# Kernel optimization log

Measured on AMD Instinct MI355X. Metric: run time of the kernel, lower is better.

Reference implementation:

```python
import jax, jax.numpy as jnp
import numpy as np


def _mlp(h, W_in, b_in, W_hid, b_hid, W_out, b_out):
    # 392 -> 1000 -> (1000)x4 -> 392, ReLU between linear layers (NICE shift net)
    h = jax.nn.relu(h @ W_in + b_in)
    for i in range(W_hid.shape[0]):  # fixed small layer count, not a data dim
        h = jax.nn.relu(h @ W_hid[i] + b_hid[i])
    return h @ W_out + b_out


def setup_inputs() -> dict:
    key = jax.random.key(0)
    ks = jax.random.split(key, 4)
    B, D, MID = 4096, 784, 1000
    half = D // 2
    return {
        "x": jax.random.normal(ks[0], (B, D), jnp.float32),
        "log_det_J": jnp.zeros((1,), jnp.float32),
        "W_in": jax.random.normal(ks[1], (half, MID), jnp.float32) * 0.05,
        "b_in": jnp.zeros((MID,), jnp.float32),
        "W_hid": jax.random.normal(ks[2], (4, MID, MID), jnp.float32) * 0.03,
        "b_hid": jnp.zeros((4, MID), jnp.float32),
        "W_out": jax.random.normal(ks[3], (MID, half), jnp.float32) * 0.03,
        "b_out": jnp.zeros((half,), jnp.float32),
    }


def reference(x, log_det_J, W_in, b_in, W_hid, b_hid, W_out, b_out):
    # mask_config = 0: first = even columns, second = odd columns
    first = x[:, 0::2]   # (B, D/2)
    second = x[:, 1::2]  # (B, D/2)
    shift = _mlp(first, W_in, b_in, W_hid, b_hid, W_out, b_out)
    y_second = second + shift  # coupling_law (reverse=False)
    # interleave: y[:, 0::2] = first, y[:, 1::2] = y_second, in one strided write
    y = jnp.stack([first, y_second], axis=2).reshape(x.shape)
    return (y, log_det_J)
```

## Files before the change

kernel.cpp:

```cpp
#include <hip/hip_runtime.h>

typedef __bf16 bf16;
typedef __bf16 bf16x8 __attribute__((ext_vector_type(8)));
typedef float f32x4 __attribute__((ext_vector_type(4)));

#define M_TOT 4096
#define D_IN  784
#define HALF  392
#define MID   1000
#define K0PAD 448
#define NPAD  1024

__device__ __forceinline__ void g2l16(const bf16* g, bf16* l) {
  __builtin_amdgcn_global_load_lds(
      (__attribute__((address_space(1))) void*)(g),
      (__attribute__((address_space(3))) void*)(l),
      16, 0, 0);
}

__device__ __forceinline__ void wtrans_tile(const float* __restrict__ W, bf16* __restrict__ WT,
                                            int K, int N, int Kpad, int tn, int tk,
                                            float (*tb)[33], int tid) {
  int n0 = tn * 32, k0 = tk * 32;
  int tx = tid & 31, ty = tid >> 5;
#pragma unroll
  for (int r = 0; r < 4; ++r) {
    int k = k0 + ty + 8 * r, n = n0 + tx;
    tb[ty + 8 * r][tx] = (k < K && n < N) ? W[(size_t)k * N + n] : 0.f;
  }
  __syncthreads();
#pragma unroll
  for (int r = 0; r < 4; ++r) {
    int n = n0 + ty + 8 * r, k = k0 + tx;
    WT[(size_t)n * Kpad + k] = (bf16)tb[tx][ty + 8 * r];
  }
}

__global__ void prep_k(const float* __restrict__ x, const float* __restrict__ ldj,
                       const float* __restrict__ W_in,
                       bf16* __restrict__ A0, bf16* __restrict__ WT0,
                       float* __restrict__ y) {
  __shared__ float tb[32][33];
  const int b = blockIdx.x, tid = threadIdx.x;
  if (b < 896) {
    int g = b * 256 + tid;
    int m = g / 56;
    int kq = g - m * 56, k0 = kq * 8;
    bf16x8 v;
    if (k0 < HALF) {
      const float4* xr = (const float4*)(x + (size_t)m * D_IN + 2 * k0);
      float4 a0 = xr[0], a1 = xr[1], a2 = xr[2], a3 = xr[3];
      v[0] = (bf16)a0.x; v[1] = (bf16)a0.z;
      v[2] = (bf16)a1.x; v[3] = (bf16)a1.z;
      v[4] = (bf16)a2.x; v[5] = (bf16)a2.z;
      v[6] = (bf16)a3.x; v[7] = (bf16)a3.z;
    } else {
#pragma unroll
      for (int j = 0; j < 8; ++j) v[j] = (bf16)0.f;
    }
    *(bf16x8*)(A0 + (size_t)m * K0PAD + k0) = v;
    if (b == 0 && tid == 0) y[(size_t)M_TOT * D_IN] = ldj[0];
    return;
  }
  int u = b - 896;
  wtrans_tile(W_in, WT0, HALF, MID, K0PAD, u & 31, u >> 5, tb, tid);
}

template <int BM, int BN, int EPI, int K>
__global__ __launch_bounds__(256, 2)
void gemm_k(const bf16* __restrict__ A, const bf16* __restrict__ BT,
            const float* __restrict__ bias, int bias_n,
            bf16* __restrict__ C,
            const float* __restrict__ x, float* __restrict__ y, int nb,
            const float* __restrict__ Wx, bf16* __restrict__ WTx,
            int wK, int wN, int wKpad, int wTN) {
  constexpr int BK = 64;
  constexpr int MT = BM / 32, NT = BN / 32;
  constexpr int KT = K / BK;
  constexpr int NBM = M_TOT / BM;
  constexpr int AI = (BM / 4) / 8;
  constexpr int BI = (BN / 4) / 8;
  constexpr int LPS = AI + BI;
  static_assert(K % BK == 0 && KT >= 2, "K/BK");
  alignas(16) __shared__ bf16 ldsA[2][BM * BK];
  alignas(16) __shared__ bf16 ldsB[2][BN * BK];
  const int tid = threadIdx.x;
  const int id = blockIdx.x;

  if (id >= nb) {
    int u = id - nb;
    wtrans_tile(Wx, WTx, wK, wN, wKpad, u % wTN, u / wTN, (float(*)[33])&ldsA[0][0], tid);
    return;
  }

  const int wave = tid >> 6, lane = tid & 63;
  const int bm = id % NBM, bn = id / NBM;

  const int srow = lane >> 3;
  const int scol = lane & 7;
  const bf16* gAb = A + ((size_t)bm * BM + wave * (BM / 4)) * K;
  const bf16* gBb = BT + ((size_t)bn * BN + wave * (BN / 4)) * K;
  const int lAo = wave * (BM / 4) * BK;
  const int lBo = wave * (BN / 4) * BK;

  const int mlane = lane & 15, quad = lane >> 4;
  const int wm = (wave & 1) * (BM / 2), wn = (wave >> 1) * (BN / 2);
  const int axor = mlane & 7;

  auto stage = [&](int kt, int pb) {
    const int koff = kt * BK;
#pragma unroll
    for (int i = 0; i < AI; ++i) {
      int r = i * 8 + srow;
      g2l16(gAb + (size_t)r * K + koff + (scol ^ (r & 7)) * 8,
            &ldsA[pb][lAo + i * 8 * BK]);
    }
#pragma unroll
    for (int i = 0; i < BI; ++i) {
      int r = i * 8 + srow;
      g2l16(gBb + (size_t)r * K + koff + (scol ^ (r & 7)) * 8,
            &ldsB[pb][lBo + i * 8 * BK]);
    }
  };

  f32x4 acc[MT][NT] = {};

  stage(0, 0);
  stage(1, 1);

  for (int kt = 0; kt < KT; ++kt) {
    const int pb = kt & 1;
    if (kt + 1 < KT)
      asm volatile("s_waitcnt vmcnt(%0)" ::"n"(LPS) : "memory");
    else
      asm volatile("s_waitcnt vmcnt(0)" ::: "memory");
    __builtin_amdgcn_s_barrier();
    __builtin_amdgcn_sched_barrier(0);

    const bf16* raB = &ldsA[pb][(wm + mlane) * BK];
    const bf16* rbB = &ldsB[pb][(wn + mlane) * BK];
    bf16x8 af[2][MT], bfr[2][NT];
#pragma unroll
    for (int s = 0; s < 2; ++s) {
      const int co = ((s * 4 + quad) ^ axor) * 8;
#pragma unroll
      for (int i = 0; i < MT; ++i) af[s][i] = *(const bf16x8*)(raB + i * 16 * BK + co);
#pragma unroll
      for (int i = 0; i < NT; ++i) bfr[s][i] = *(const bf16x8*)(rbB + i * 16 * BK + co);
    }
    asm volatile("s_waitcnt lgkmcnt(0)" ::: "memory");
    __builtin_amdgcn_sched_barrier(0);
    __builtin_amdgcn_s_barrier();
    __builtin_amdgcn_sched_barrier(0);

    if (kt + 2 < KT) stage(kt + 2, pb);

#pragma unroll
    for (int s = 0; s < 2; ++s)
#pragma unroll
      for (int mt = 0; mt < MT; ++mt)
#pragma unroll
        for (int nt = 0; nt < NT; ++nt)
          acc[mt][nt] = __builtin_amdgcn_mfma_f32_16x16x32_bf16(
              af[s][mt], bfr[s][nt], acc[mt][nt], 0, 0, 0);
  }

  const int ng0 = bn * BN + wn + mlane;
  const int mg0 = bm * BM + wm + quad * 4;

  if (EPI == 0) {
    float bv[NT];
#pragma unroll
    for (int nt = 0; nt < NT; ++nt) {
      int n = ng0 + nt * 16;
      bv[nt] = (n < bias_n) ? bias[n] : 0.f;
    }
#pragma unroll
    for (int mt = 0; mt < MT; ++mt)
#pragma unroll
      for (int nt = 0; nt < NT; ++nt)
#pragma unroll
        for (int r = 0; r < 4; ++r) {
          int m = mg0 + mt * 16 + r;
          int n = ng0 + nt * 16;
          float v = fmaxf(acc[mt][nt][r] + bv[nt], 0.f);
          C[(size_t)m * NPAD + n] = (bf16)v;
        }
  } else {
    const float2* x2 = (const float2*)x;
    float2* y2 = (float2*)y;
#pragma unroll
    for (int nt = 0; nt < NT; ++nt) {
      int n = ng0 + nt * 16;
      if (n < HALF) {
        float bb = bias[n];
#pragma unroll
        for (int mt = 0; mt < MT; ++mt)
#pragma unroll
          for (int r = 0; r < 4; ++r) {
            int m = mg0 + mt * 16 + r;
            size_t off = (size_t)m * (D_IN / 2) + n;
            float2 v = x2[off];
            v.y += acc[mt][nt][r] + bb;
            y2[off] = v;
          }
      }
    }
  }
}

extern "C" void kernel_launch(void* const* d_in, const int* in_sizes, int n_in,
                              void* d_out, int out_size, void* d_ws, size_t ws_size,
                              hipStream_t stream) {
  const float* x     = (const float*)d_in[0];
  const float* ldj   = (const float*)d_in[1];
  const float* W_in  = (const float*)d_in[2];
  const float* b_in  = (const float*)d_in[3];
  const float* W_hid = (const float*)d_in[4];
  const float* b_hid = (const float*)d_in[5];
  const float* W_out = (const float*)d_in[6];
  const float* b_out = (const float*)d_in[7];
  float* y = (float*)d_out;

  char* p = (char*)d_ws;
  bf16* A0  = (bf16*)(p + 0);
  bf16* H0  = (bf16*)(p + 3670016);
  bf16* H1  = (bf16*)(p + 12058624);
  bf16* WT0 = (bf16*)(p + 20447232);
  bf16* WTh = (bf16*)(p + 21364736);
  bf16* WT5 = (bf16*)(p + 29753344);

  const size_t WH = (size_t)NPAD * NPAD;
  const size_t WS = (size_t)MID * MID;

  prep_k<<<dim3(896 + 448), 256, 0, stream>>>(x, ldj, W_in, A0, WT0, y);

  gemm_k<128, 64, 0, K0PAD><<<dim3(512 + 1024), 256, 0, stream>>>(
      A0, WT0, b_in, MID, H0, nullptr, nullptr, 512,
      W_hid + 0 * WS, WTh + 0 * WH, MID, MID, NPAD, 32);
  gemm_k<128, 64, 0, NPAD><<<dim3(512 + 1024), 256, 0, stream>>>(
      H0, WTh + 0 * WH, b_hid + 0 * MID, MID, H1, nullptr, nullptr, 512,
      W_hid + 1 * WS, WTh + 1 * WH, MID, MID, NPAD, 32);
  gemm_k<128, 64, 0, NPAD><<<dim3(512 + 1024), 256, 0, stream>>>(
      H1, WTh + 1 * WH, b_hid + 1 * MID, MID, H0, nullptr, nullptr, 512,
      W_hid + 2 * WS, WTh + 2 * WH, MID, MID, NPAD, 32);
  gemm_k<128, 64, 0, NPAD><<<dim3(512 + 1024), 256, 0, stream>>>(
      H0, WTh + 2 * WH, b_hid + 2 * MID, MID, H1, nullptr, nullptr, 512,
      W_hid + 3 * WS, WTh + 3 * WH, MID, MID, NPAD, 32);
  gemm_k<128, 64, 0, NPAD><<<dim3(512 + 512), 256, 0, stream>>>(
      H1, WTh + 3 * WH, b_hid + 3 * MID, MID, H0, nullptr, nullptr, 512,
      W_out, WT5, MID, HALF, NPAD, 16);
  gemm_k<64, 64, 1, NPAD><<<dim3(512), 256, 0, stream>>>(
      H0, WT5, b_out, HALF, nullptr, x, y, 512,
      nullptr, nullptr, 0, 0, 0, 1);
}
```

Measured before the change: 170.5 us.

## Move weight transposes into prep kernel, use 128x128 tiles with 4-stage pipeline

All weight transpose/convert work now runs in the prep kernel instead of being hidden in extra blocks of each GEMM launch. The GEMM is specialised to 128x128 tiles with four LDS buffers and explicit vmcnt waits for deeper prefetch, and the launch_bounds occupancy hint is dropped. This raises per-tile data reuse and the amount of load latency hidden, but leaves only 256 (or 128 for the last layer) blocks per GEMM on a 256-CU device and uses 128 KB of LDS per block. It also serialises all transposes ahead of the first GEMM instead of overlapping them with GEMM work.

Result: slower. 187.1 us (+9.7%).

```diff
diff --git a/kernel.cpp b/kernel.cpp
--- a/kernel.cpp
+++ b/kernel.cpp
@@ -37,8 +37,10 @@
 }
 
 __global__ void prep_k(const float* __restrict__ x, const float* __restrict__ ldj,
-                       const float* __restrict__ W_in,
+                       const float* __restrict__ W_in, const float* __restrict__ W_hid,
+                       const float* __restrict__ W_out,
                        bf16* __restrict__ A0, bf16* __restrict__ WT0,
+                       bf16* __restrict__ WTh, bf16* __restrict__ WT5,
                        float* __restrict__ y) {
   __shared__ float tb[32][33];
   const int b = blockIdx.x, tid = threadIdx.x;
@@ -62,36 +64,44 @@
     if (b == 0 && tid == 0) y[(size_t)M_TOT * D_IN] = ldj[0];
     return;
   }
-  int u = b - 896;
-  wtrans_tile(W_in, WT0, HALF, MID, K0PAD, u & 31, u >> 5, tb, tid);
-}
-
-template <int BM, int BN, int EPI, int K>
-__global__ __launch_bounds__(256, 2)
+  int t = b - 896;
+  const float* W; bf16* WT; int K, N, Kpad, tn, tk;
+  if (t < 448) {
+    W = W_in; WT = WT0; K = HALF; N = MID; Kpad = K0PAD;
+    tn = t & 31; tk = t >> 5;
+  } else if (t < 4544) {
+    int u = t - 448; int i = u >> 10; u &= 1023;
+    W = W_hid + (size_t)i * MID * MID; WT = WTh + (size_t)i * NPAD * NPAD;
+    K = MID; N = MID; Kpad = NPAD;
+    tn = u & 31; tk = u >> 5;
+  } else {
+    int u = t - 4544;
+    W = W_out; WT = WT5; K = MID; N = HALF; Kpad = NPAD;
+    tn = u & 15; tk = u >> 4;
+  }
+  wtrans_tile(W, WT, K, N, Kpad, tn, tk, tb, tid);
+}
+
+template <int EPI, int K>
+__global__ __launch_bounds__(256)
 void gemm_k(const bf16* __restrict__ A, const bf16* __restrict__ BT,
             const float* __restrict__ bias, int bias_n,
             bf16* __restrict__ C,
-            const float* __restrict__ x, float* __restrict__ y, int nb,
-            const float* __restrict__ Wx, bf16* __restrict__ WTx,
-            int wK, int wN, int wKpad, int wTN) {
-  constexpr int BK = 64;
+            const float* __restrict__ x, float* __restrict__ y) {
+  constexpr int BM = 128, BN = 128, BK = 64, NBUF = 4;
   constexpr int MT = BM / 32, NT = BN / 32;
   constexpr int KT = K / BK;
   constexpr int NBM = M_TOT / BM;
   constexpr int AI = (BM / 4) / 8;
   constexpr int BI = (BN / 4) / 8;
   constexpr int LPS = AI + BI;
-  static_assert(K % BK == 0 && KT >= 2, "K/BK");
-  alignas(16) __shared__ bf16 ldsA[2][BM * BK];
-  alignas(16) __shared__ bf16 ldsB[2][BN * BK];
+  static_assert(K % BK == 0 && KT >= NBUF, "K/BK");
+  static_assert(LPS == 8, "vmcnt immediates assume LPS=8");
+
+  alignas(16) __shared__ bf16 ldsA[NBUF][BM * BK];
+  alignas(16) __shared__ bf16 ldsB[NBUF][BN * BK];
   const int tid = threadIdx.x;
   const int id = blockIdx.x;
-
-  if (id >= nb) {
-    int u = id - nb;
-    wtrans_tile(Wx, WTx, wK, wN, wKpad, u % wTN, u / wTN, (float(*)[33])&ldsA[0][0], tid);
-    return;
-  }
 
   const int wave = tid >> 6, lane = tid & 63;
   const int bm = id % NBM, bn = id / NBM;
@@ -125,13 +135,17 @@
 
   f32x4 acc[MT][NT] = {};
 
-  stage(0, 0);
-  stage(1, 1);
+  stage(0, 0); stage(1, 1); stage(2, 2); stage(3, 3);
 
   for (int kt = 0; kt < KT; ++kt) {
-    const int pb = kt & 1;
-    if (kt + 1 < KT)
-      asm volatile("s_waitcnt vmcnt(%0)" ::"n"(LPS) : "memory");
+    const int pb = kt & 3;
+    const int rem = KT - 1 - kt;
+    if (rem >= 3)
+      asm volatile("s_waitcnt vmcnt(24)" ::: "memory");
+    else if (rem == 2)
+      asm volatile("s_waitcnt vmcnt(16)" ::: "memory");
+    else if (rem == 1)
+      asm volatile("s_waitcnt vmcnt(8)" ::: "memory");
     else
       asm volatile("s_waitcnt vmcnt(0)" ::: "memory");
     __builtin_amdgcn_s_barrier();
@@ -153,7 +167,7 @@
     __builtin_amdgcn_s_barrier();
     __builtin_amdgcn_sched_barrier(0);
 
-    if (kt + 2 < KT) stage(kt + 2, pb);
+    if (kt + NBUF < KT) stage(kt + NBUF, pb);
 
 #pragma unroll
     for (int s = 0; s < 2; ++s)
@@ -231,26 +245,14 @@
   bf16* WT5 = (bf16*)(p + 29753344);
 
   const size_t WH = (size_t)NPAD * NPAD;
-  const size_t WS = (size_t)MID * MID;
-
-  prep_k<<<dim3(896 + 448), 256, 0, stream>>>(x, ldj, W_in, A0, WT0, y);
-
-  gemm_k<128, 64, 0, K0PAD><<<dim3(512 + 1024), 256, 0, stream>>>(
-      A0, WT0, b_in, MID, H0, nullptr, nullptr, 512,
-      W_hid + 0 * WS, WTh + 0 * WH, MID, MID, NPAD, 32);
-  gemm_k<128, 64, 0, NPAD><<<dim3(512 + 1024), 256, 0, stream>>>(
-      H0, WTh + 0 * WH, b_hid + 0 * MID, MID, H1, nullptr, nullptr, 512,
-      W_hid + 1 * WS, WTh + 1 * WH, MID, MID, NPAD, 32);
-  gemm_k<128, 64, 0, NPAD><<<dim3(512 + 1024), 256, 0, stream>>>(
-      H1, WTh + 1 * WH, b_hid + 1 * MID, MID, H0, nullptr, nullptr, 512,
-      W_hid + 2 * WS, WTh + 2 * WH, MID, MID, NPAD, 32);
-  gemm_k<128, 64, 0, NPAD><<<dim3(512 + 1024), 256, 0, stream>>>(
-      H0, WTh + 2 * WH, b_hid + 2 * MID, MID, H1, nullptr, nullptr, 512,
-      W_hid + 3 * WS, WTh + 3 * WH, MID, MID, NPAD, 32);
-  gemm_k<128, 64, 0, NPAD><<<dim3(512 + 512), 256, 0, stream>>>(
-      H1, WTh + 3 * WH, b_hid + 3 * MID, MID, H0, nullptr, nullptr, 512,
-      W_out, WT5, MID, HALF, NPAD, 16);
-  gemm_k<64, 64, 1, NPAD><<<dim3(512), 256, 0, stream>>>(
-      H0, WT5, b_out, HALF, nullptr, x, y, 512,
-      nullptr, nullptr, 0, 0, 0, 1);
-}
+
+  prep_k<<<dim3(896 + 5056), 256, 0, stream>>>(x, ldj, W_in, W_hid, W_out,
+                                               A0, WT0, WTh, WT5, y);
+
+  gemm_k<0, K0PAD><<<dim3(256), 256, 0, stream>>>(A0, WT0, b_in, MID, H0, nullptr, nullptr);
+  gemm_k<0, NPAD><<<dim3(256), 256, 0, stream>>>(H0, WTh + 0 * WH, b_hid + 0 * MID, MID, H1, nullptr, nullptr);
+  gemm_k<0, NPAD><<<dim3(256), 256, 0, stream>>>(H1, WTh + 1 * WH, b_hid + 1 * MID, MID, H0, nullptr, nullptr);
+  gemm_k<0, NPAD><<<dim3(256), 256, 0, stream>>>(H0, WTh + 2 * WH, b_hid + 2 * MID, MID, H1, nullptr, nullptr);
+  gemm_k<0, NPAD><<<dim3(256), 256, 0, stream>>>(H1, WTh + 3 * WH, b_hid + 3 * MID, MID, H0, nullptr, nullptr);
+  gemm_k<1, NPAD><<<dim3(128), 256, 0, stream>>>(H0, WT5, b_out, HALF, nullptr, x, y);
+}
```

## Split GEMM blocks into producer and consumer waves with MFMA priority

Applied to the files above, without the earlier changes.

Each GEMM block now has 512 threads: four waves issue global-to-LDS loads and four waves do the LDS reads and MFMAs, with s_setprio raised around the MFMA loop. The aim is to overlap memory traffic with compute by specialising waves instead of having every wave do both. The last layer now also uses 128x64 tiles, so it launches half as many blocks, and the weight-transpose helper is rewritten for 512-thread blocks. The cost is extra barrier coordination, idle producer waves during the epilogue, and lower occupancy for the final small GEMM.

Measured after the change: 174.0 us. +2.1%, slower.

```diff
diff --git a/kernel.cpp b/kernel.cpp
--- a/kernel.cpp
+++ b/kernel.cpp
@@ -33,6 +33,24 @@
   for (int r = 0; r < 4; ++r) {
     int n = n0 + ty + 8 * r, k = k0 + tx;
     WT[(size_t)n * Kpad + k] = (bf16)tb[tx][ty + 8 * r];
+  }
+}
+
+__device__ __forceinline__ void wtrans_tile512(const float* __restrict__ W, bf16* __restrict__ WT,
+                                               int K, int N, int Kpad, int tn, int tk,
+                                               float (*tb)[33], int tid) {
+  int n0 = tn * 32, k0 = tk * 32;
+  int tx = tid & 31, ty = (tid >> 5) & 15;
+#pragma unroll
+  for (int r = 0; r < 2; ++r) {
+    int k = k0 + ty + 16 * r, n = n0 + tx;
+    tb[ty + 16 * r][tx] = (k < K && n < N) ? W[(size_t)k * N + n] : 0.f;
+  }
+  __syncthreads();
+#pragma unroll
+  for (int r = 0; r < 2; ++r) {
+    int n = n0 + ty + 16 * r, k = k0 + tx;
+    WT[(size_t)n * Kpad + k] = (bf16)tb[tx][ty + 16 * r];
   }
 }
 
@@ -66,22 +84,20 @@
   wtrans_tile(W_in, WT0, HALF, MID, K0PAD, u & 31, u >> 5, tb, tid);
 }
 
-template <int BM, int BN, int EPI, int K>
-__global__ __launch_bounds__(256, 2)
+template <int EPI, int K>
+__global__ __launch_bounds__(512, 4)
 void gemm_k(const bf16* __restrict__ A, const bf16* __restrict__ BT,
             const float* __restrict__ bias, int bias_n,
             bf16* __restrict__ C,
             const float* __restrict__ x, float* __restrict__ y, int nb,
             const float* __restrict__ Wx, bf16* __restrict__ WTx,
             int wK, int wN, int wKpad, int wTN) {
-  constexpr int BK = 64;
+  constexpr int BM = 128, BN = 64, BK = 64;
   constexpr int MT = BM / 32, NT = BN / 32;
   constexpr int KT = K / BK;
   constexpr int NBM = M_TOT / BM;
-  constexpr int AI = (BM / 4) / 8;
-  constexpr int BI = (BN / 4) / 8;
-  constexpr int LPS = AI + BI;
   static_assert(K % BK == 0 && KT >= 2, "K/BK");
+
   alignas(16) __shared__ bf16 ldsA[2][BM * BK];
   alignas(16) __shared__ bf16 ldsB[2][BN * BK];
   const int tid = threadIdx.x;
@@ -89,81 +105,91 @@
 
   if (id >= nb) {
     int u = id - nb;
-    wtrans_tile(Wx, WTx, wK, wN, wKpad, u % wTN, u / wTN, (float(*)[33])&ldsA[0][0], tid);
+    wtrans_tile512(Wx, WTx, wK, wN, wKpad, u % wTN, u / wTN,
+                   (float(*)[33])&ldsA[0][0], tid);
     return;
   }
 
   const int wave = tid >> 6, lane = tid & 63;
+  const bool producer = (wave >= 4);
   const int bm = id % NBM, bn = id / NBM;
 
+  const int p = wave - 4;
   const int srow = lane >> 3;
   const int scol = lane & 7;
-  const bf16* gAb = A + ((size_t)bm * BM + wave * (BM / 4)) * K;
-  const bf16* gBb = BT + ((size_t)bn * BN + wave * (BN / 4)) * K;
-  const int lAo = wave * (BM / 4) * BK;
-  const int lBo = wave * (BN / 4) * BK;
+  const bf16* gAb = A + ((size_t)bm * BM + p * 32) * K;
+  const bf16* gBb = BT + ((size_t)bn * BN + p * 16) * K;
+
+  auto stage = [&](int kt, int pb) {
+    const int koff = kt * BK;
+#pragma unroll
+    for (int i = 0; i < 4; ++i) {
+      int r = i * 8 + srow;
+      g2l16(gAb + (size_t)r * K + koff + (scol ^ (r & 7)) * 8,
+            &ldsA[pb][(p * 32 + i * 8) * BK]);
+    }
+#pragma unroll
+    for (int i = 0; i < 2; ++i) {
+      int r = i * 8 + srow;
+      g2l16(gBb + (size_t)r * K + koff + (scol ^ (r & 7)) * 8,
+            &ldsB[pb][(p * 16 + i * 8) * BK]);
+    }
+  };
 
   const int mlane = lane & 15, quad = lane >> 4;
   const int wm = (wave & 1) * (BM / 2), wn = (wave >> 1) * (BN / 2);
   const int axor = mlane & 7;
 
-  auto stage = [&](int kt, int pb) {
-    const int koff = kt * BK;
-#pragma unroll
-    for (int i = 0; i < AI; ++i) {
-      int r = i * 8 + srow;
-      g2l16(gAb + (size_t)r * K + koff + (scol ^ (r & 7)) * 8,
-            &ldsA[pb][lAo + i * 8 * BK]);
-    }
-#pragma unroll
-    for (int i = 0; i < BI; ++i) {
-      int r = i * 8 + srow;
-      g2l16(gBb + (size_t)r * K + koff + (scol ^ (r & 7)) * 8,
-            &ldsB[pb][lBo + i * 8 * BK]);
-    }
-  };
-
   f32x4 acc[MT][NT] = {};
 
-  stage(0, 0);
-  stage(1, 1);
+  if (producer) { stage(0, 0); stage(1, 1); }
 
   for (int kt = 0; kt < KT; ++kt) {
     const int pb = kt & 1;
-    if (kt + 1 < KT)
-      asm volatile("s_waitcnt vmcnt(%0)" ::"n"(LPS) : "memory");
-    else
-      asm volatile("s_waitcnt vmcnt(0)" ::: "memory");
+    if (producer) {
+      if (kt + 1 < KT)
+        asm volatile("s_waitcnt vmcnt(6)" ::: "memory");
+      else
+        asm volatile("s_waitcnt vmcnt(0)" ::: "memory");
+    }
     __builtin_amdgcn_s_barrier();
     __builtin_amdgcn_sched_barrier(0);
 
-    const bf16* raB = &ldsA[pb][(wm + mlane) * BK];
-    const bf16* rbB = &ldsB[pb][(wn + mlane) * BK];
     bf16x8 af[2][MT], bfr[2][NT];
-#pragma unroll
-    for (int s = 0; s < 2; ++s) {
-      const int co = ((s * 4 + quad) ^ axor) * 8;
-#pragma unroll
-      for (int i = 0; i < MT; ++i) af[s][i] = *(const bf16x8*)(raB + i * 16 * BK + co);
-#pragma unroll
-      for (int i = 0; i < NT; ++i) bfr[s][i] = *(const bf16x8*)(rbB + i * 16 * BK + co);
-    }
-    asm volatile("s_waitcnt lgkmcnt(0)" ::: "memory");
-    __builtin_amdgcn_sched_barrier(0);
+    if (!producer) {
+      const bf16* raB = &ldsA[pb][(wm + mlane) * BK];
+      const bf16* rbB = &ldsB[pb][(wn + mlane) * BK];
+#pragma unroll
+      for (int s = 0; s < 2; ++s) {
+        const int co = ((s * 4 + quad) ^ axor) * 8;
+#pragma unroll
+        for (int i = 0; i < MT; ++i) af[s][i] = *(const bf16x8*)(raB + i * 16 * BK + co);
+#pragma unroll
+        for (int i = 0; i < NT; ++i) bfr[s][i] = *(const bf16x8*)(rbB + i * 16 * BK + co);
+      }
+      asm volatile("s_waitcnt lgkmcnt(0)" ::: "memory");
+      __builtin_amdgcn_sched_barrier(0);
+    }
     __builtin_amdgcn_s_barrier();
     __builtin_amdgcn_sched_barrier(0);
 
-    if (kt + 2 < KT) stage(kt + 2, pb);
-
-#pragma unroll
-    for (int s = 0; s < 2; ++s)
-#pragma unroll
-      for (int mt = 0; mt < MT; ++mt)
-#pragma unroll
-        for (int nt = 0; nt < NT; ++nt)
-          acc[mt][nt] = __builtin_amdgcn_mfma_f32_16x16x32_bf16(
-              af[s][mt], bfr[s][nt], acc[mt][nt], 0, 0, 0);
-  }
+    if (producer) {
+      if (kt + 2 < KT) stage(kt + 2, pb);
+    } else {
+      __builtin_amdgcn_s_setprio(1);
+#pragma unroll
+      for (int s = 0; s < 2; ++s)
+#pragma unroll
+        for (int mt = 0; mt < MT; ++mt)
+#pragma unroll
+          for (int nt = 0; nt < NT; ++nt)
+            acc[mt][nt] = __builtin_amdgcn_mfma_f32_16x16x32_bf16(
+                af[s][mt], bfr[s][nt], acc[mt][nt], 0, 0, 0);
+      __builtin_amdgcn_s_setprio(0);
+    }
+  }
+
+  if (producer) return;
 
   const int ng0 = bn * BN + wn + mlane;
   const int mg0 = bm * BM + wm + quad * 4;
@@ -235,22 +261,22 @@
 
   prep_k<<<dim3(896 + 448), 256, 0, stream>>>(x, ldj, W_in, A0, WT0, y);
 
-  gemm_k<128, 64, 0, K0PAD><<<dim3(512 + 1024), 256, 0, stream>>>(
+  gemm_k<0, K0PAD><<<dim3(512 + 1024), 512, 0, stream>>>(
       A0, WT0, b_in, MID, H0, nullptr, nullptr, 512,
       W_hid + 0 * WS, WTh + 0 * WH, MID, MID, NPAD, 32);
-  gemm_k<128, 64, 0, NPAD><<<dim3(512 + 1024), 256, 0, stream>>>(
+  gemm_k<0, NPAD><<<dim3(512 + 1024), 512, 0, stream>>>(
       H0, WTh + 0 * WH, b_hid + 0 * MID, MID, H1, nullptr, nullptr, 512,
       W_hid + 1 * WS, WTh + 1 * WH, MID, MID, NPAD, 32);
-  gemm_k<128, 64, 0, NPAD><<<dim3(512 + 1024), 256, 0, stream>>>(
+  gemm_k<0, NPAD><<<dim3(512 + 1024), 512, 0, stream>>>(
       H1, WTh + 1 * WH, b_hid + 1 * MID, MID, H0, nullptr, nullptr, 512,
       W_hid + 2 * WS, WTh + 2 * WH, MID, MID, NPAD, 32);
-  gemm_k<128, 64, 0, NPAD><<<dim3(512 + 1024), 256, 0, stream>>>(
+  gemm_k<0, NPAD><<<dim3(512 + 1024), 512, 0, stream>>>(
       H0, WTh + 2 * WH, b_hid + 2 * MID, MID, H1, nullptr, nullptr, 512,
       W_hid + 3 * WS, WTh + 3 * WH, MID, MID, NPAD, 32);
-  gemm_k<128, 64, 0, NPAD><<<dim3(512 + 512), 256, 0, stream>>>(
+  gemm_k<0, NPAD><<<dim3(512 + 512), 512, 0, stream>>>(
       H1, WTh + 3 * WH, b_hid + 3 * MID, MID, H0, nullptr, nullptr, 512,
       W_out, WT5, MID, HALF, NPAD, 16);
-  gemm_k<64, 64, 1, NPAD><<<dim3(512), 256, 0, stream>>>(
-      H0, WT5, b_out, HALF, nullptr, x, y, 512,
+  gemm_k<1, NPAD><<<dim3(256), 512, 0, stream>>>(
+      H0, WT5, b_out, HALF, nullptr, x, y, 256,
       nullptr, nullptr, 0, 0, 0, 1);
 }
```
